# Optimization experiments

Hardware: AMD Instinct MI355X
Metric: run time of the kernel (lower is better)

Reference implementation:

```python
import jax, jax.numpy as jnp
import numpy as np

N_FINE = 400000
N_COARSE = 100000
E_POOL = 1200000
E_CONV = 1600000
E_UNPOOL = 1200000
C = 64


def setup_inputs() -> dict:
    key = jax.random.key(0)
    ks = jax.random.split(key, 16)
    s = 1.0 / np.sqrt(C)
    return {
        "x": jax.random.normal(ks[0], (N_FINE, C), dtype=jnp.float32),
        "W1_root": jax.random.normal(ks[1], (C, C), dtype=jnp.float32) * s,
        "W1_nb": jax.random.normal(ks[2], (C, C), dtype=jnp.float32) * s,
        "b1": jax.random.normal(ks[3], (C,), dtype=jnp.float32) * s,
        "W2_root": jax.random.normal(ks[4], (C, C), dtype=jnp.float32) * s,
        "W2_nb": jax.random.normal(ks[5], (C, C), dtype=jnp.float32) * s,
        "b2": jax.random.normal(ks[6], (C,), dtype=jnp.float32) * s,
        "pool_src": jax.random.randint(ks[7], (E_POOL,), 0, N_FINE),
        "pool_dst": jax.random.randint(ks[8], (E_POOL,), 0, N_COARSE),
        "pool_attr": jax.random.uniform(ks[9], (E_POOL, 1), dtype=jnp.float32),
        "conv_src": jax.random.randint(ks[10], (E_CONV,), 0, N_COARSE),
        "conv_dst": jax.random.randint(ks[11], (E_CONV,), 0, N_COARSE),
        "conv_attr": jax.random.uniform(ks[12], (E_CONV, 1), dtype=jnp.float32),
        "unpool_src": jax.random.randint(ks[13], (E_UNPOOL,), 0, N_COARSE),
        "unpool_dst": jax.random.randint(ks[14], (E_UNPOOL,), 0, N_FINE),
        "unpool_attr": jax.random.uniform(ks[15], (E_UNPOOL, 1), dtype=jnp.float32),
        "n_coarse": N_COARSE,
        "n_fine": N_FINE,
    }


def reference(x, W1_root, W1_nb, b1, W2_root, W2_nb, b2,
              pool_src, pool_dst, pool_attr,
              conv_src, conv_dst, conv_attr,
              unpool_src, unpool_dst, unpool_attr,
              n_coarse, n_fine):
    # CustomPoolingAdd: weighted scatter-add fine -> coarse
    xc = jax.ops.segment_sum(x[pool_src] * pool_attr, pool_dst,
                             num_segments=n_coarse)  # [n_coarse, C]

    # CustomGraphConvPointPoint: h_i' = W_root h_i + b + sum_j w_ij * (W_nb h_j)
    def conv(h, Wr, Wn, b):
        msg = jax.ops.segment_sum((h @ Wn)[conv_src] * conv_attr, conv_dst,
                                  num_segments=n_coarse)
        return h @ Wr + msg + b

    h = conv(xc, W1_root, W1_nb, b1)
    h = conv(h, W2_root, W2_nb, b2)

    # CustomUnpooling: weighted scatter-add coarse -> fine
    out = jax.ops.segment_sum(h[unpool_src] * unpool_attr, unpool_dst,
                              num_segments=n_fine)  # [n_fine, C]
    return out
```

## Files before the change

kernel.cpp:

```cpp
#include <hip/hip_runtime.h>


#define NCH 64


__global__ __launch_bounds__(256) void hist_kernel(const int* __restrict__ dst,
                                                   int* __restrict__ cnt,
                                                   int nE) {
  int e = blockIdx.x * blockDim.x + threadIdx.x;
  if (e < nE) atomicAdd(&cnt[dst[e]], 1);
}

static __device__ __forceinline__ int wave_incl_scan(int v, int lane) {
#pragma unroll
  for (int off = 1; off < 64; off <<= 1) {
    int t = __shfl_up(v, off, 64);
    if (lane >= off) v += t;
  }
  return v;
}

__global__ __launch_bounds__(256) void scan_reduce(const int* __restrict__ cnt,
                                                   int* __restrict__ bsums,
                                                   int n) {
  int base = blockIdx.x * 2048 + threadIdx.x * 8;
  int s = 0;
#pragma unroll
  for (int j = 0; j < 8; ++j) {
    int idx = base + j;
    s += (idx < n) ? cnt[idx] : 0;
  }
  int lane = threadIdx.x & 63;
  int w = threadIdx.x >> 6;
#pragma unroll
  for (int off = 32; off; off >>= 1) s += __shfl_xor(s, off, 64);
  __shared__ int ws_[4];
  if (lane == 0) ws_[w] = s;
  __syncthreads();
  if (threadIdx.x == 0) bsums[blockIdx.x] = ws_[0] + ws_[1] + ws_[2] + ws_[3];
}

__global__ void scan_bsums(int* __restrict__ bs, int nB) {
  int lane = threadIdx.x;
  int carry = 0;
  for (int base = 0; base < nB; base += 64) {
    int i = base + lane;
    int orig = (i < nB) ? bs[i] : 0;
    int v = wave_incl_scan(orig, lane);
    if (i < nB) bs[i] = v - orig + carry;
    carry += __shfl(v, 63, 64);
  }
}

__global__ __launch_bounds__(256) void scan_final(int* __restrict__ cnt_rowptr,
                                                  const int* __restrict__ bsums,
                                                  int n) {
  int base = blockIdx.x * 2048 + threadIdx.x * 8;
  int v[8];
  int s = 0;
#pragma unroll
  for (int j = 0; j < 8; ++j) {
    int idx = base + j;
    v[j] = (idx < n) ? cnt_rowptr[idx] : 0;
    s += v[j];
  }
  int lane = threadIdx.x & 63;
  int w = threadIdx.x >> 6;
  int inc = wave_incl_scan(s, lane);
  __shared__ int wsum[4];
  if (lane == 63) wsum[w] = inc;
  __syncthreads();
  int woff = 0;
  for (int ww = 0; ww < w; ++ww) woff += wsum[ww];
  int excl = inc - s + woff + bsums[blockIdx.x];
#pragma unroll
  for (int j = 0; j < 8; ++j) {
    int idx = base + j;
    if (idx <= n) cnt_rowptr[idx] = excl;
    excl += v[j];
  }
}

__global__ __launch_bounds__(256) void permute_kernel(
    const int* __restrict__ src, const int* __restrict__ dst,
    const float* __restrict__ attr, int* __restrict__ cursor,
    int2* __restrict__ payload, int nE) {
  int e = blockIdx.x * blockDim.x + threadIdx.x;
  if (e >= nE) return;
  int p = atomicAdd(&cursor[dst[e]], 1);
  payload[p] = make_int2(src[e], __float_as_int(attr[e]));
}

__global__ __launch_bounds__(256) void gather4_kernel(
    const float* __restrict__ in, const int* __restrict__ rowptr,
    const int2* __restrict__ payload, float* __restrict__ out, int nDst) {
  const int wid = (blockIdx.x * blockDim.x + threadIdx.x) >> 6;
  const int lane = threadIdx.x & 63;
  if (wid >= nDst) return;
  const int beg = rowptr[wid];
  const int end = rowptr[wid + 1];
  const int g = lane >> 4;
  const int cq = (lane & 15) * 4;

  float4 acc = make_float4(0.f, 0.f, 0.f, 0.f);
  const int2 z = make_int2(0, 0);
  for (int jb = beg; jb < end; jb += 16) {
    const int j0 = jb + g, j1 = j0 + 4, j2 = j0 + 8, j3 = j0 + 12;
    int2 p0 = (j0 < end) ? payload[j0] : z;
    int2 p1 = (j1 < end) ? payload[j1] : z;
    int2 p2 = (j2 < end) ? payload[j2] : z;
    int2 p3 = (j3 < end) ? payload[j3] : z;
    float4 v0 = *(const float4*)(in + (size_t)p0.x * NCH + cq);
    float4 v1 = *(const float4*)(in + (size_t)p1.x * NCH + cq);
    float4 v2 = *(const float4*)(in + (size_t)p2.x * NCH + cq);
    float4 v3 = *(const float4*)(in + (size_t)p3.x * NCH + cq);
    const float a0 = __int_as_float(p0.y), a1 = __int_as_float(p1.y);
    const float a2 = __int_as_float(p2.y), a3 = __int_as_float(p3.y);
    acc.x = __builtin_fmaf(v0.x, a0, acc.x);
    acc.y = __builtin_fmaf(v0.y, a0, acc.y);
    acc.z = __builtin_fmaf(v0.z, a0, acc.z);
    acc.w = __builtin_fmaf(v0.w, a0, acc.w);
    acc.x = __builtin_fmaf(v1.x, a1, acc.x);
    acc.y = __builtin_fmaf(v1.y, a1, acc.y);
    acc.z = __builtin_fmaf(v1.z, a1, acc.z);
    acc.w = __builtin_fmaf(v1.w, a1, acc.w);
    acc.x = __builtin_fmaf(v2.x, a2, acc.x);
    acc.y = __builtin_fmaf(v2.y, a2, acc.y);
    acc.z = __builtin_fmaf(v2.z, a2, acc.z);
    acc.w = __builtin_fmaf(v2.w, a2, acc.w);
    acc.x = __builtin_fmaf(v3.x, a3, acc.x);
    acc.y = __builtin_fmaf(v3.y, a3, acc.y);
    acc.z = __builtin_fmaf(v3.z, a3, acc.z);
    acc.w = __builtin_fmaf(v3.w, a3, acc.w);
  }
#pragma unroll
  for (int off = 16; off <= 32; off <<= 1) {
    acc.x += __shfl_xor(acc.x, off, 64);
    acc.y += __shfl_xor(acc.y, off, 64);
    acc.z += __shfl_xor(acc.z, off, 64);
    acc.w += __shfl_xor(acc.w, off, 64);
  }
  if (g == 0) *(float4*)(out + (size_t)wid * NCH + cq) = acc;
}

__global__ __launch_bounds__(256) void node_gemm2_kernel(
    const float* __restrict__ h, const float* __restrict__ g,
    const float* __restrict__ Wr, const float* __restrict__ Wn,
    const float* __restrict__ bias, float* __restrict__ out, int n) {
  const int lane = threadIdx.x & 63;

  float wr[64], wn[64];
#pragma unroll
  for (int k = 0; k < 64; ++k) {
    wr[k] = Wr[k * NCH + lane];
    wn[k] = Wn[k * NCH + lane];
  }
  const float bv = bias[lane];

  const int wave = (blockIdx.x * blockDim.x + threadIdx.x) >> 6;
  const int nwaves = (gridDim.x * blockDim.x) >> 6;

  for (int i = wave; i < n; i += nwaves) {
    float hv = h[(size_t)i * NCH + lane];
    float gv = g[(size_t)i * NCH + lane];
    float acc = bv;
#pragma unroll
    for (int k = 0; k < 64; ++k) {
      acc = __builtin_fmaf(
          __uint_as_float(__builtin_amdgcn_readlane(__float_as_uint(hv), k)),
          wr[k], acc);
      acc = __builtin_fmaf(
          __uint_as_float(__builtin_amdgcn_readlane(__float_as_uint(gv), k)),
          wn[k], acc);
    }
    out[(size_t)i * NCH + lane] = acc;
  }
}

extern "C" void kernel_launch(void* const* d_in, const int* in_sizes, int n_in,
                              void* d_out, int out_size, void* d_ws,
                              size_t ws_size, hipStream_t stream) {
  const float* x = (const float*)d_in[0];
  const float* W1r = (const float*)d_in[1];
  const float* W1n = (const float*)d_in[2];
  const float* b1 = (const float*)d_in[3];
  const float* W2r = (const float*)d_in[4];
  const float* W2n = (const float*)d_in[5];
  const float* b2 = (const float*)d_in[6];
  const int* pool_src = (const int*)d_in[7];
  const int* pool_dst = (const int*)d_in[8];
  const float* pool_attr = (const float*)d_in[9];
  const int* conv_src = (const int*)d_in[10];
  const int* conv_dst = (const int*)d_in[11];
  const float* conv_attr = (const float*)d_in[12];
  const int* unpool_src = (const int*)d_in[13];
  const int* unpool_dst = (const int*)d_in[14];
  const float* unpool_attr = (const float*)d_in[15];

  const int Ep = in_sizes[7];
  const int Ec = in_sizes[10];
  const int Eu = in_sizes[13];
  const int NC = 100000;
  const int NF = 400000;

  const size_t MiB = 1024u * 1024u;

  char* ws = (char*)d_ws;
  float* bufA = (float*)ws;
  int* up_rp = (int*)(ws + 26 * MiB);
  int2* up_pl = (int2*)(ws + 28 * MiB);

  char* ob = (char*)d_out;
  float* bufB = (float*)ob;
  float* bufC = (float*)(ob + 26 * MiB);
  int* cv_rp = (int*)(ob + 52 * MiB);
  int2* cv_pl = (int2*)(ob + 53 * MiB);
  int* pl_rp = (int*)(ob + 66 * MiB);
  int2* pl_pl = (int2*)(ob + 67 * MiB);
  int* cursor = (int*)(ob + 77 * MiB);
  int* bsums = (int*)(ob + 79 * MiB);

  const dim3 blk(256);

  auto build_csr = [&](const int* srcA, const int* dstA, const float* attrA,
                       int nE, int nDst, int* rp, int2* pl) {
    int nB = (nDst + 1 + 2047) / 2048;
    hipMemsetAsync(rp, 0, (size_t)(nDst + 1) * sizeof(int), stream);
    hist_kernel<<<dim3((nE + 255) / 256), blk, 0, stream>>>(dstA, rp, nE);
    scan_reduce<<<dim3(nB), blk, 0, stream>>>(rp, bsums, nDst);
    scan_bsums<<<dim3(1), dim3(64), 0, stream>>>(bsums, nB);
    scan_final<<<dim3(nB), blk, 0, stream>>>(rp, bsums, nDst);
    hipMemcpyAsync(cursor, rp, (size_t)nDst * sizeof(int),
                   hipMemcpyDeviceToDevice, stream);
    permute_kernel<<<dim3((nE + 255) / 256), blk, 0, stream>>>(
        srcA, dstA, attrA, cursor, pl, nE);
  };

  build_csr(pool_src, pool_dst, pool_attr, Ep, NC, pl_rp, pl_pl);
  build_csr(conv_src, conv_dst, conv_attr, Ec, NC, cv_rp, cv_pl);
  build_csr(unpool_src, unpool_dst, unpool_attr, Eu, NF, up_rp, up_pl);

  const int gemm_grid = 2048;
  const dim3 gNC((NC + 3) / 4), gNF((NF + 3) / 4);

  gather4_kernel<<<gNC, blk, 0, stream>>>(x, pl_rp, pl_pl, bufA, NC);

  gather4_kernel<<<gNC, blk, 0, stream>>>(bufA, cv_rp, cv_pl, bufB, NC);
  node_gemm2_kernel<<<dim3(gemm_grid), blk, 0, stream>>>(bufA, bufB, W1r, W1n,
                                                         b1, bufC, NC);

  gather4_kernel<<<gNC, blk, 0, stream>>>(bufC, cv_rp, cv_pl, bufB, NC);
  node_gemm2_kernel<<<dim3(gemm_grid), blk, 0, stream>>>(bufC, bufB, W2r, W2n,
                                                         b2, bufA, NC);

  gather4_kernel<<<gNF, blk, 0, stream>>>(bufA, up_rp, up_pl, (float*)d_out,
                                          NF);
}
```

Before: 1.050 ms.

## Record atomic rank during histogram to remove second atomic pass in CSR build

The histogram kernel now stores the atomicAdd return value as each edge's rank within its destination bucket. The placement kernel then computes the slot as rowptr[dst]+rank, with no atomics and no cursor copy. Both kernels also process four edges per thread using vector loads. This removes one atomic pass and a device-to-device memcpy per CSR build, at the cost of writing and reading an extra rank array.

```diff
diff --git a/kernel.cpp b/kernel.cpp
--- a/kernel.cpp
+++ b/kernel.cpp
@@ -4,11 +4,21 @@
 #define NCH 64
 
 
-__global__ __launch_bounds__(256) void hist_kernel(const int* __restrict__ dst,
-                                                   int* __restrict__ cnt,
-                                                   int nE) {
-  int e = blockIdx.x * blockDim.x + threadIdx.x;
-  if (e < nE) atomicAdd(&cnt[dst[e]], 1);
+__global__ __launch_bounds__(256) void hist_rank_kernel(
+    const int* __restrict__ dst, int* __restrict__ cnt, int* __restrict__ rank,
+    int nE) {
+  int t = blockIdx.x * blockDim.x + threadIdx.x;
+  int e0 = t * 4;
+  if (e0 + 3 < nE) {
+    int4 d = *(const int4*)(dst + e0);
+    int r0 = atomicAdd(&cnt[d.x], 1);
+    int r1 = atomicAdd(&cnt[d.y], 1);
+    int r2 = atomicAdd(&cnt[d.z], 1);
+    int r3 = atomicAdd(&cnt[d.w], 1);
+    *(int4*)(rank + e0) = make_int4(r0, r1, r2, r3);
+  } else {
+    for (int e = e0; e < nE; ++e) rank[e] = atomicAdd(&cnt[dst[e]], 1);
+  }
 }
 
 static __device__ __forceinline__ int wave_incl_scan(int v, int lane) {
@@ -81,14 +91,26 @@
   }
 }
 
-__global__ __launch_bounds__(256) void permute_kernel(
+__global__ __launch_bounds__(256) void place_kernel(
     const int* __restrict__ src, const int* __restrict__ dst,
-    const float* __restrict__ attr, int* __restrict__ cursor,
-    int2* __restrict__ payload, int nE) {
-  int e = blockIdx.x * blockDim.x + threadIdx.x;
-  if (e >= nE) return;
-  int p = atomicAdd(&cursor[dst[e]], 1);
-  payload[p] = make_int2(src[e], __float_as_int(attr[e]));
+    const float* __restrict__ attr, const int* __restrict__ rp,
+    const int* __restrict__ rank, int2* __restrict__ payload, int nE) {
+  int t = blockIdx.x * blockDim.x + threadIdx.x;
+  int e0 = t * 4;
+  if (e0 + 3 < nE) {
+    int4 s = *(const int4*)(src + e0);
+    int4 d = *(const int4*)(dst + e0);
+    float4 a = *(const float4*)(attr + e0);
+    int4 r = *(const int4*)(rank + e0);
+    payload[rp[d.x] + r.x] = make_int2(s.x, __float_as_int(a.x));
+    payload[rp[d.y] + r.y] = make_int2(s.y, __float_as_int(a.y));
+    payload[rp[d.z] + r.z] = make_int2(s.z, __float_as_int(a.z));
+    payload[rp[d.w] + r.w] = make_int2(s.w, __float_as_int(a.w));
+  } else {
+    for (int e = e0; e < nE; ++e)
+      payload[rp[dst[e]] + rank[e]] =
+          make_int2(src[e], __float_as_int(attr[e]));
+  }
 }
 
 __global__ __launch_bounds__(256) void gather4_kernel(
@@ -217,23 +239,23 @@
   int2* cv_pl = (int2*)(ob + 53 * MiB);
   int* pl_rp = (int*)(ob + 66 * MiB);
   int2* pl_pl = (int2*)(ob + 67 * MiB);
-  int* cursor = (int*)(ob + 77 * MiB);
-  int* bsums = (int*)(ob + 79 * MiB);
+  int* rank = (int*)(ob + 77 * MiB);
+  int* bsums = (int*)(ob + 84 * MiB);
 
   const dim3 blk(256);
 
   auto build_csr = [&](const int* srcA, const int* dstA, const float* attrA,
                        int nE, int nDst, int* rp, int2* pl) {
     int nB = (nDst + 1 + 2047) / 2048;
+    int nT4 = (nE + 3) / 4;
     hipMemsetAsync(rp, 0, (size_t)(nDst + 1) * sizeof(int), stream);
-    hist_kernel<<<dim3((nE + 255) / 256), blk, 0, stream>>>(dstA, rp, nE);
+    hist_rank_kernel<<<dim3((nT4 + 255) / 256), blk, 0, stream>>>(dstA, rp,
+                                                                  rank, nE);
     scan_reduce<<<dim3(nB), blk, 0, stream>>>(rp, bsums, nDst);
     scan_bsums<<<dim3(1), dim3(64), 0, stream>>>(bsums, nB);
     scan_final<<<dim3(nB), blk, 0, stream>>>(rp, bsums, nDst);
-    hipMemcpyAsync(cursor, rp, (size_t)nDst * sizeof(int),
-                   hipMemcpyDeviceToDevice, stream);
-    permute_kernel<<<dim3((nE + 255) / 256), blk, 0, stream>>>(
-        srcA, dstA, attrA, cursor, pl, nE);
+    place_kernel<<<dim3((nT4 + 255) / 256), blk, 0, stream>>>(
+        srcA, dstA, attrA, rp, rank, pl, nE);
   };
 
   build_csr(pool_src, pool_dst, pool_attr, Ep, NC, pl_rp, pl_pl);
```

New measurement: 876.9 us. 16.5% less time.
